# Optimization experiments

Measured on AMD Instinct MI355X. Metric: run time of the kernel, lower is better.

Reference implementation:

```python
import jax, jax.numpy as jnp
import numpy as np

B, N = 32, 196                  # batch, tokens (14x14 patches on all 4 scales)
CN = (64, 128, 256, 512)        # per-branch channel dims
H = 4                           # attention heads
KV = sum(CN)                    # 960
EPS = 1e-5                      # InstanceNorm2d default eps (affine=False)


def setup_inputs() -> dict:
    key = jax.random.key(0)
    ks = jax.random.split(key, 16)
    inp = {}
    for i, c in enumerate(CN):
        inp[f"emb{i+1}"] = jax.random.normal(ks[i], (B, N, c), dtype=jnp.float32)
    inp["emb_all"] = jnp.concatenate([inp[f"emb{i+1}"] for i in range(4)], axis=2)
    # per-head query weights (one Linear per head, bias=False): [H, out, in]
    for i, c in enumerate(CN):
        inp[f"Wq{i+1}"] = 0.02 * jax.random.normal(ks[4 + i], (H, c, c), dtype=jnp.float32)
    inp["Wk"] = 0.02 * jax.random.normal(ks[8], (H, KV, KV), dtype=jnp.float32)
    inp["Wv"] = 0.02 * jax.random.normal(ks[9], (H, KV, KV), dtype=jnp.float32)
    for i, c in enumerate(CN):
        inp[f"Wo{i+1}"] = 0.02 * jax.random.normal(ks[10 + i], (c, c), dtype=jnp.float32)
    return inp


def _branch(emb, Wq, K, V):
    # emb: [B,N,C], Wq: [H,C,C] -> Q^T: [B,H,C,N] (stack heads, transpose(-1,-2))
    Qt = jnp.einsum('bnd,hcd->bhcn', emb, Wq)
    # scores: [B,H,C,KV], scaled by sqrt(KV_size)
    s = jnp.einsum('bhcn,bhnk->bhck', Qt, K) * (1.0 / np.sqrt(KV))
    # InstanceNorm2d over spatial dims (C,KV) per (batch, head), no affine
    m = jnp.mean(s, axis=(2, 3), keepdims=True)
    v = jnp.var(s, axis=(2, 3), keepdims=True)
    s = (s - m) * jax.lax.rsqrt(v + EPS)
    p = jax.nn.softmax(s, axis=-1)              # softmax over KV dim (dim=3)
    # context = probs @ V^T -> [B,H,C,N]; permute(0,3,2,1).mean(dim=3) == mean over heads
    ctx = jnp.einsum('bhck,bhnk->bnc', p, V) / H  # [B,N,C]
    return ctx


def reference(emb1, emb2, emb3, emb4, emb_all,
              Wq1, Wq2, Wq3, Wq4, Wk, Wv, Wo1, Wo2, Wo3, Wo4):
    # per-head K/V projections of concatenated embedding: [B,H,N,KV]
    K = jnp.einsum('bnk,hok->bhno', emb_all, Wk)
    V = jnp.einsum('bnk,hok->bhno', emb_all, Wv)
    O1 = _branch(emb1, Wq1, K, V) @ Wo1.T
    O2 = _branch(emb2, Wq2, K, V) @ Wo2.T
    O3 = _branch(emb3, Wq3, K, V) @ Wo3.T
    O4 = _branch(emb4, Wq4, K, V) @ Wo4.T
    return (O1, O2, O3, O4)
```

## Files before the change

kernel.cpp:

```cpp
#include <hip/hip_runtime.h>
#include <math.h>

typedef __attribute__((ext_vector_type(8))) short bf16x8;
typedef __attribute__((ext_vector_type(4))) float f32x4;
typedef unsigned short u16;

__device__ __forceinline__ u16 f2bf(float f) {
  unsigned u = __float_as_uint(f);
  return (u16)((u + 0x7FFFu + ((u >> 16) & 1u)) >> 16);
}
__device__ __forceinline__ float bf2f(u16 h) {
  return __uint_as_float(((unsigned)h) << 16);
}

__device__ __forceinline__ void gload16(const u16* g, void* lds) {
  __builtin_amdgcn_global_load_lds(
      (const __attribute__((address_space(1))) unsigned int*)g,
      (__attribute__((address_space(3))) unsigned int*)lds, 16, 0, 0);
}

__device__ __forceinline__ void mfma_core(
    const u16* __restrict__ A, int lda,
    const u16* __restrict__ B, int ldb,
    int K, f32x4 (&acc)[4][4], u16* As, u16* Bs)
{
  const int tid = threadIdx.x;
  const int l = tid & 63, w = tid >> 6;
  const int srow = w * 16 + (l >> 2);
  const int kel  = (l & 3) * 8;
  char* AsB = (char*)As + w * 1024;
  char* BsB = (char*)Bs + w * 1024;
  const u16* Ap  = A + (size_t)srow * lda + kel;
  const u16* Ap2 = A + (size_t)(srow + 64) * lda + kel;
  const u16* Bp  = B + (size_t)srow * ldb + kel;
  const u16* Bp2 = B + (size_t)(srow + 64) * ldb + kel;
  const int wm = w >> 1, wn = w & 1;
  const int aoff = (wm * 64 + (l & 15)) * 32 + (l >> 4) * 8;
  const int boff = (wn * 64 + (l & 15)) * 32 + (l >> 4) * 8;
  for (int kb = 0; kb < K; kb += 32) {
    __syncthreads();
    gload16(Ap + kb,  AsB);
    gload16(Ap2 + kb, AsB + 4096);
    gload16(Bp + kb,  BsB);
    gload16(Bp2 + kb, BsB + 4096);
    __syncthreads();
    bf16x8 av[4], bv[4];
#pragma unroll
    for (int i = 0; i < 4; ++i) {
      av[i] = *(const bf16x8*)(As + aoff + i * 16 * 32);
      bv[i] = *(const bf16x8*)(Bs + boff + i * 16 * 32);
    }
#pragma unroll
    for (int i = 0; i < 4; ++i)
#pragma unroll
      for (int j = 0; j < 4; ++j)
        acc[i][j] = __builtin_amdgcn_mfma_f32_16x16x32_bf16(av[i], bv[j], acc[i][j], 0, 0, 0);
  }
}

__global__ __launch_bounds__(256) void k_cvt(
    const float* __restrict__ eall,
    const float* __restrict__ Wq1, const float* __restrict__ Wq2,
    const float* __restrict__ Wq3, const float* __restrict__ Wq4,
    const float* __restrict__ Wk, const float* __restrict__ Wv,
    const float* __restrict__ Wo1, const float* __restrict__ Wo2,
    const float* __restrict__ Wo3, const float* __restrict__ Wo4,
    u16* __restrict__ embA, u16* __restrict__ WkB, u16* __restrict__ WvB,
    u16* __restrict__ WqB, u16* __restrict__ WoB)
{
  long long idx = (long long)blockIdx.x * 256 + threadIdx.x;
  const float* src; u16* dst; int srcR, dstR, C; long long stride, off, loc;
  if (idx < 6881280LL)       { loc = idx;               src=eall; dst=embA; srcR=196; dstR=224;  C=960; stride=215040; off=0; }
  else if (idx < 10813440LL) { loc = idx - 6881280LL;   src=Wk;   dst=WkB;  srcR=960; dstR=1024; C=960; stride=983040; off=0; }
  else if (idx < 14745600LL) { loc = idx - 10813440LL;  src=Wv;   dst=WvB;  srcR=960; dstR=1024; C=960; stride=983040; off=0; }
  else if (idx < 14778368LL) { loc = idx - 14745600LL;  src=Wq1;  dst=WqB;  srcR=64;  dstR=128;  C=64;  stride=352256; off=0; }
  else if (idx < 14843904LL) { loc = idx - 14778368LL;  src=Wq2;  dst=WqB;  srcR=128; dstR=128;  C=128; stride=352256; off=8192; }
  else if (idx < 15106048LL) { loc = idx - 14843904LL;  src=Wq3;  dst=WqB;  srcR=256; dstR=256;  C=256; stride=352256; off=24576; }
  else if (idx < 16154624LL) { loc = idx - 15106048LL;  src=Wq4;  dst=WqB;  srcR=512; dstR=512;  C=512; stride=352256; off=90112; }
  else if (idx < 16162816LL) { loc = idx - 16154624LL;  src=Wo1;  dst=WoB;  srcR=64;  dstR=128;  C=64;  stride=0; off=0; }
  else if (idx < 16179200LL) { loc = idx - 16162816LL;  src=Wo2;  dst=WoB;  srcR=128; dstR=128;  C=128; stride=0; off=8192; }
  else if (idx < 16244736LL) { loc = idx - 16179200LL;  src=Wo3;  dst=WoB;  srcR=256; dstR=256;  C=256; stride=0; off=24576; }
  else if (idx < 16506880LL) { loc = idx - 16244736LL;  src=Wo4;  dst=WoB;  srcR=512; dstR=512;  C=512; stride=0; off=90112; }
  else return;
  const long long per = (long long)dstR * C;
  const int g = (int)(loc / per);
  const int r2 = (int)(loc % per);
  const int rr = r2 / C, c = r2 - rr * C;
  const float v = (rr < srcR) ? src[((long long)g * srcR + rr) * C + c] : 0.f;
  dst[g * stride + off + (long long)rr * C + c] = f2bf(v);
}

__global__ __launch_bounds__(256) void k_kt(const u16* __restrict__ embA,
    const u16* __restrict__ WkB, u16* __restrict__ Kt, int b0, int NB)
{
  __shared__ u16 As[128 * 32], Bs[128 * 32];
  const int h = blockIdx.z;
  const int m0 = blockIdx.y * 128, n0 = blockIdx.x * 128;
  const u16* A = WkB + (size_t)h * 1024 * 960 + (size_t)m0 * 960;
  const u16* B = embA + (size_t)(b0 * 224 + n0) * 960;
  f32x4 acc[4][4] = {};
  mfma_core(A, 960, B, 960, 960, acc, As, Bs);
  const int tid = threadIdx.x, l = tid & 63, w = tid >> 6, wm = w >> 1, wn = w & 1;
  u16* C = Kt + (size_t)h * 1024 * NB;
#pragma unroll
  for (int i = 0; i < 4; ++i) {
    const int gm0 = m0 + wm * 64 + i * 16 + (l >> 4) * 4;
#pragma unroll
    for (int j = 0; j < 4; ++j) {
      const int n = n0 + wn * 64 + j * 16 + (l & 15);
#pragma unroll
      for (int r = 0; r < 4; ++r)
        C[(size_t)(gm0 + r) * NB + n] = f2bf(acc[i][j][r]);
    }
  }
}

__global__ __launch_bounds__(256) void k_v(const u16* __restrict__ embA,
    const u16* __restrict__ WvB, u16* __restrict__ V, int b0, int NB)
{
  __shared__ u16 As[128 * 32], Bs[128 * 32];
  const int h = blockIdx.z;
  const int m0 = blockIdx.y * 128, n0 = blockIdx.x * 128;
  const u16* A = embA + (size_t)(b0 * 224 + m0) * 960;
  const u16* B = WvB + (size_t)h * 1024 * 960 + (size_t)n0 * 960;
  f32x4 acc[4][4] = {};
  mfma_core(A, 960, B, 960, 960, acc, As, Bs);
  const int tid = threadIdx.x, l = tid & 63, w = tid >> 6, wm = w >> 1, wn = w & 1;
#pragma unroll
  for (int i = 0; i < 4; ++i) {
    const int t0 = m0 + wm * 64 + i * 16 + (l >> 4) * 4;
#pragma unroll
    for (int r = 0; r < 4; ++r) {
      const int t = t0 + r;
      const int lb = t / 224, n = t - lb * 224;
      u16* C = V + ((size_t)(lb * 4 + h) * 256 + n) * 1024;
#pragma unroll
      for (int j = 0; j < 4; ++j) {
        const int col = n0 + wn * 64 + j * 16 + (l & 15);
        C[col] = f2bf(acc[i][j][r]);
      }
    }
  }
}

__global__ __launch_bounds__(256) void k_q(const u16* __restrict__ embA,
    const u16* __restrict__ WqB, u16* __restrict__ Qt, int b0, int NB)
{
  __shared__ u16 As[128 * 32], Bs[128 * 32];
  const int h = blockIdx.z;
  const int y = blockIdx.y;
  const int br = (y == 0) ? 0 : (y == 1) ? 1 : (y < 4) ? 2 : 3;
  const int mt = (y <= 1) ? 0 : (y < 4) ? (y - 2) : (y - 4);
  const int Ci = 64 << br;
  const int coff = (br == 0) ? 0 : (br == 1) ? 64 : (br == 2) ? 192 : 448;
  const int wqo = (br == 0) ? 0 : (br == 1) ? 8192 : (br == 2) ? 24576 : 90112;
  const int n0 = blockIdx.x * 128;
  const u16* A = WqB + (size_t)h * 352256 + wqo + (size_t)mt * 128 * Ci;
  const u16* B = embA + (size_t)(b0 * 224 + n0) * 960 + coff;
  f32x4 acc[4][4] = {};
  mfma_core(A, Ci, B, 960, Ci, acc, As, Bs);
  const int tid = threadIdx.x, l = tid & 63, w = tid >> 6, wm = w >> 1, wn = w & 1;
  u16* C = Qt + (size_t)h * 1024 * NB;
#pragma unroll
  for (int i = 0; i < 4; ++i) {
    const int lr0 = mt * 128 + wm * 64 + i * 16 + (l >> 4) * 4;
#pragma unroll
    for (int j = 0; j < 4; ++j) {
      const int n = n0 + wn * 64 + j * 16 + (l & 15);
#pragma unroll
      for (int r = 0; r < 4; ++r)
        if (lr0 + r < Ci)
          C[(size_t)(coff + lr0 + r) * NB + n] = f2bf(acc[i][j][r]);
    }
  }
}

#define TS_LD 72
__global__ __launch_bounds__(256) void k_gk(const u16* __restrict__ Kt,
                                            u16* __restrict__ Gk, int NB)
{
  __shared__ u16 TsA[128 * TS_LD], TsB[128 * TS_LD];
  const int z = blockIdx.z, lb = z >> 2, h = z & 3;
  const int n0a = blockIdx.y * 96, n0b = blockIdx.x * 96;
  const u16* Kz = Kt + (size_t)h * 1024 * NB + lb * 224;
  const int tid = threadIdx.x, l = tid & 63, w = tid >> 6, wm = w >> 1, wn = w & 1;
  f32x4 acc[4][4] = {};
  for (int o0 = 0; o0 < 1024; o0 += 64) {
    __syncthreads();
#pragma unroll
    for (int it = 0; it < 16; ++it) {
      const int e = it * 256 + tid;
      const int o = e >> 6, np = e & 63;
      const unsigned va = *(const unsigned*)(Kz + (size_t)(o0 + o) * NB + n0a + np * 2);
      const unsigned vb = *(const unsigned*)(Kz + (size_t)(o0 + o) * NB + n0b + np * 2);
      const int o8 = o >> 3, oe = o & 7;
      const int r0 = np * 2, r1 = r0 + 1;
      TsA[r0 * TS_LD + (((o8 ^ (r0 & 7)) << 3) | oe)] = (u16)(va & 0xffff);
      TsA[r1 * TS_LD + (((o8 ^ (r1 & 7)) << 3) | oe)] = (u16)(va >> 16);
      TsB[r0 * TS_LD + (((o8 ^ (r0 & 7)) << 3) | oe)] = (u16)(vb & 0xffff);
      TsB[r1 * TS_LD + (((o8 ^ (r1 & 7)) << 3) | oe)] = (u16)(vb >> 16);
    }
    __syncthreads();
#pragma unroll
    for (int ks = 0; ks < 2; ++ks) {
      bf16x8 av[4], bv[4];
#pragma unroll
      for (int i = 0; i < 4; ++i) {
        const int ra = wm * 64 + i * 16 + (l & 15);
        av[i] = *(const bf16x8*)(TsA + ra * TS_LD + (((ks * 4 + (l >> 4)) ^ (ra & 7)) << 3));
        const int rb = wn * 64 + i * 16 + (l & 15);
        bv[i] = *(const bf16x8*)(TsB + rb * TS_LD + (((ks * 4 + (l >> 4)) ^ (rb & 7)) << 3));
      }
#pragma unroll
      for (int i = 0; i < 4; ++i)
#pragma unroll
        for (int j = 0; j < 4; ++j)
          acc[i][j] = __builtin_amdgcn_mfma_f32_16x16x32_bf16(av[i], bv[j], acc[i][j], 0, 0, 0);
    }
  }
  u16* G = Gk + (size_t)z * 256 * 224;
#pragma unroll
  for (int i = 0; i < 4; ++i) {
    const int ra0 = n0a + wm * 64 + i * 16 + (l >> 4) * 4;
#pragma unroll
    for (int j = 0; j < 4; ++j) {
      const int cb = n0b + wn * 64 + j * 16 + (l & 15);
#pragma unroll
      for (int r = 0; r < 4; ++r)
        G[(size_t)(ra0 + r) * 224 + cb] = f2bf(acc[i][j][r]);
    }
  }
}

__global__ __launch_bounds__(256) void k_qgq(const u16* __restrict__ Qt,
    const u16* __restrict__ Gk, float* __restrict__ stats, int NB)
{
  __shared__ u16 As[128 * 32], Bs[128 * 32];
  __shared__ float sb[4];
  const int z = blockIdx.z, lb = z >> 2, h = z & 3;
  const int m0 = blockIdx.y * 128;
  const int tx = blockIdx.x;
  const int tid = threadIdx.x;
  if (tid < 4) sb[tid] = 0.f;
  const u16* A = Qt + (size_t)h * 1024 * NB + (size_t)m0 * NB + lb * 224;
  const u16* B = Gk + (size_t)z * 256 * 224 + (size_t)(tx * 96) * 224;
  f32x4 acc[4][4] = {};
  mfma_core(A, NB, B, 224, 224, acc, As, Bs);
  const int l = tid & 63, w = tid >> 6, wm = w >> 1, wn = w & 1;
  const u16* Qbase = Qt + (size_t)h * 1024 * NB + lb * 224;
  float part[4]; int pbr[4]; bool ok[4];
#pragma unroll
  for (int i = 0; i < 4; ++i) {
    const int gm0 = m0 + wm * 64 + i * 16 + (l >> 4) * 4;
    pbr[i] = (gm0 < 64) ? 0 : (gm0 < 192) ? 1 : (gm0 < 448) ? 2 : 3;
    ok[i] = (gm0 < 960);
    float s = 0.f;
    if (ok[i]) {
#pragma unroll
      for (int j = 0; j < 4; ++j) {
        const int col = tx * 96 + wn * 64 + j * 16 + (l & 15);
        if (tx == 1 && col < 128) continue;
#pragma unroll
        for (int r = 0; r < 4; ++r)
          s += acc[i][j][r] * bf2f(Qbase[(size_t)(gm0 + r) * NB + col]);
      }
    }
    part[i] = s;
  }
  __syncthreads();
#pragma unroll
  for (int i = 0; i < 4; ++i)
    if (ok[i]) atomicAdd(&sb[pbr[i]], part[i]);
  __syncthreads();
  if (tid < 4) atomicAdd(stats + (size_t)z * 4 + tid, sb[tid]);
}

__global__ __launch_bounds__(256, 2) void k_att(
    const u16* __restrict__ Qt, const u16* __restrict__ Kt,
    const u16* __restrict__ V, const float* __restrict__ stats,
    u16* __restrict__ ctxh, int NB)
{
  __shared__ u16 smem[39744];
  __shared__ float rsum[64];

  const int z = blockIdx.x, ct = blockIdx.y;
  const int lb = z >> 2, h = z & 3;
  const int c0 = ct * 64;
  const int tid = threadIdx.x, l = tid & 63, w = tid >> 6;
  const int wm = w >> 1, wn = w & 1;
  const int br = (c0 < 64) ? 0 : (c0 < 192) ? 1 : (c0 < 448) ? 2 : 3;
  const float scale = 0.03227486121839514f;
  const float cnt = (float)(64 << br) * 960.f;
  const float var = stats[(size_t)z * 4 + br] * scale * scale / cnt;
  const float cs = scale * rsqrtf(var + 1e-5f);

  const u16* Qz = Qt + (size_t)h * 1024 * NB + (size_t)c0 * NB + lb * 224;
  const u16* Kz = Kt + (size_t)h * 1024 * NB + lb * 224;
  const u16* Vz = V + (size_t)z * 256 * 1024;

  bf16x8 qa[2][7];
#pragma unroll
  for (int i = 0; i < 2; ++i)
#pragma unroll
    for (int ks = 0; ks < 7; ++ks)
      qa[i][ks] = *(const bf16x8*)(Qz + (size_t)(wm * 32 + i * 16 + (l & 15)) * NB
                                   + ks * 32 + (l >> 4) * 8);
  if (tid < 64) rsum[tid] = 0.f;

  const u16* kp[4];
#pragma unroll
  for (int c = 0; c < 4; ++c) {
    const int e = (c * 4 + w) * 512 + l * 8;
    const int row = e / 232, col = e - row * 232;
    kp[c] = Kz + (size_t)row * NB + col;
  }
  const u16* vp[5];
#pragma unroll
  for (int c = 0; c < 5; ++c) {
    const int e = (c * 4 + w) * 512 + l * 8;
    const int row = e / 40, col = e - row * 40;
    vp[c] = Vz + (size_t)row * 1024 + col;
  }
  u16* Ps = smem + 37184;

#pragma unroll
  for (int c = 0; c < 4; ++c) { gload16(kp[c], (char*)(smem) + (c * 4 + w) * 1024); kp[c] += (size_t)32 * NB; }
#pragma unroll
  for (int c = 0; c < 5; ++c) { gload16(vp[c], (char*)(smem + 16704) + (c * 4 + w) * 1024); vp[c] += 32; }
  __syncthreads();

  f32x4 cacc[7][2] = {};
  float rp[2][4] = {};
  int cur = 0;

  for (int oc = 0; oc < 30; ++oc) {
    const int koff = cur ? 8352 : 0;
    const int voff = cur ? 26944 : 16704;
    const int koff2 = cur ? 0 : 8352;
    const int voff2 = cur ? 16704 : 26944;
    if (oc < 29) {
#pragma unroll
      for (int c = 0; c < 4; ++c) { gload16(kp[c], (char*)(smem + koff2) + (c * 4 + w) * 1024); kp[c] += (size_t)32 * NB; }
#pragma unroll
      for (int c = 0; c < 5; ++c) { gload16(vp[c], (char*)(smem + voff2) + (c * 4 + w) * 1024); vp[c] += 32; }
    }
    const u16* Ks = smem + koff;
    const u16* Vs = smem + voff;
    f32x4 sacc[2] = {};
#pragma unroll
    for (int ks = 0; ks < 7; ++ks) {
      const bf16x8 kb = *(const bf16x8*)(Ks + (wn * 16 + (l & 15)) * 232 + ks * 32 + (l >> 4) * 8);
#pragma unroll
      for (int i = 0; i < 2; ++i)
        sacc[i] = __builtin_amdgcn_mfma_f32_16x16x32_bf16(qa[i][ks], kb, sacc[i], 0, 0, 0);
    }
#pragma unroll
    for (int i = 0; i < 2; ++i)
#pragma unroll
      for (int r = 0; r < 4; ++r) {
        const float p = __expf(sacc[i][r] * cs);
        rp[i][r] += p;
        Ps[(wm * 32 + i * 16 + (l >> 4) * 4 + r) * 40 + wn * 16 + (l & 15)] = f2bf(p);
      }
    asm volatile("s_waitcnt lgkmcnt(0)" ::: "memory");
    __builtin_amdgcn_s_barrier();
    __builtin_amdgcn_sched_barrier(0);
    bf16x8 pv[2];
#pragma unroll
    for (int j = 0; j < 2; ++j)
      pv[j] = *(const bf16x8*)(Ps + (wn * 32 + j * 16 + (l & 15)) * 40 + (l >> 4) * 8);
#pragma unroll
    for (int i2 = 0; i2 < 7; ++i2) {
      const bf16x8 av = *(const bf16x8*)(Vs + (wm * 112 + i2 * 16 + (l & 15)) * 40 + (l >> 4) * 8);
#pragma unroll
      for (int j = 0; j < 2; ++j)
        cacc[i2][j] = __builtin_amdgcn_mfma_f32_16x16x32_bf16(av, pv[j], cacc[i2][j], 0, 0, 0);
    }
    asm volatile("s_waitcnt vmcnt(0) lgkmcnt(0)" ::: "memory");
    __builtin_amdgcn_s_barrier();
    __builtin_amdgcn_sched_barrier(0);
    cur ^= 1;
  }
#pragma unroll
  for (int i = 0; i < 2; ++i)
#pragma unroll
    for (int r = 0; r < 4; ++r) {
      float v = rp[i][r];
      v += __shfl_xor(v, 1); v += __shfl_xor(v, 2);
      v += __shfl_xor(v, 4); v += __shfl_xor(v, 8);
      if ((l & 15) == 0) atomicAdd(&rsum[wm * 32 + i * 16 + (l >> 4) * 4 + r], v);
    }
  __syncthreads();
  float inv[2];
#pragma unroll
  for (int j = 0; j < 2; ++j)
    inv[j] = 1.f / rsum[wn * 32 + j * 16 + (l & 15)];

  u16* Cs = smem;
  u16* dst = ctxh + (size_t)z * 229376 + c0;
#pragma unroll
  for (int pass = 0; pass < 2; ++pass) {
    __syncthreads();
    if (wm == pass) {
#pragma unroll
      for (int i2 = 0; i2 < 7; ++i2)
#pragma unroll
        for (int j = 0; j < 2; ++j)
#pragma unroll
          for (int r = 0; r < 4; ++r)
            Cs[(i2 * 16 + (l >> 4) * 4 + r) * 72 + wn * 32 + j * 16 + (l & 15)]
                = f2bf(cacc[i2][j][r] * inv[j]);
    }
    __syncthreads();
    for (int u = tid; u < 112 * 8; u += 256) {
      const int row = u >> 3, c8 = u & 7;
      *(uint4*)(dst + (size_t)(pass * 112 + row) * 1024 + c8 * 8) =
          *(const uint4*)(Cs + row * 72 + c8 * 8);
    }
  }
}

__global__ __launch_bounds__(256) void k_ctxred(const u16* __restrict__ ctxh,
    u16* __restrict__ ctx, int Bc)
{
  const long long i8 = ((long long)blockIdx.x * 256 + threadIdx.x) * 8;
  if (i8 >= (long long)Bc * 229376) return;
  const int lb = (int)(i8 / 229376);
  const int off = (int)(i8 - (long long)lb * 229376);
  const u16* p = ctxh + (size_t)lb * 4 * 229376 + off;
  float s[8] = {};
#pragma unroll
  for (int h = 0; h < 4; ++h) {
    bf16x8 v = *(const bf16x8*)(p + (size_t)h * 229376);
#pragma unroll
    for (int i = 0; i < 8; ++i) s[i] += bf2f((u16)v[i]);
  }
  bf16x8 o;
#pragma unroll
  for (int i = 0; i < 8; ++i) o[i] = (short)f2bf(s[i] * 0.25f);
  *(bf16x8*)(ctx + (size_t)lb * 262144 + off) = o;
}

__global__ __launch_bounds__(256) void k_o(const u16* __restrict__ ctx,
    const u16* __restrict__ WoB, float* __restrict__ out, int b0)
{
  __shared__ u16 As[128 * 32], Bs[128 * 32];
  const int lb = blockIdx.z;
  const int x = blockIdx.x;
  const int br = (x == 0) ? 0 : (x == 1) ? 1 : (x < 4) ? 2 : 3;
  const int nt = (x <= 1) ? 0 : (x < 4) ? (x - 2) : (x - 4);
  const int Ci = 64 << br;
  const int coff = (br == 0) ? 0 : (br == 1) ? 64 : (br == 2) ? 192 : 448;
  const int woo = (br == 0) ? 0 : (br == 1) ? 8192 : (br == 2) ? 24576 : 90112;
  const long long ob = (br == 0) ? 0LL : (br == 1) ? 401408LL : (br == 2) ? 1204224LL : 2809856LL;
  const int m0 = blockIdx.y * 128;
  const u16* A = ctx + (size_t)lb * 262144 + (size_t)m0 * 1024 + coff;
  const u16* B = WoB + woo + (size_t)nt * 128 * Ci;
  f32x4 acc[4][4] = {};
  mfma_core(A, 1024, B, Ci, Ci, acc, As, Bs);
  const int tid = threadIdx.x, l = tid & 63, w = tid >> 6, wm = w >> 1, wn = w & 1;
  float* O = out + ob;
  const int gb = b0 + lb;
#pragma unroll
  for (int i = 0; i < 4; ++i) {
    const int row0 = m0 + wm * 64 + i * 16 + (l >> 4) * 4;
#pragma unroll
    for (int j = 0; j < 4; ++j) {
      const int cg = nt * 128 + wn * 64 + j * 16 + (l & 15);
#pragma unroll
      for (int r = 0; r < 4; ++r) {
        const int row = row0 + r;
        if (row < 196 && cg < Ci)
          O[((size_t)gb * 196 + row) * Ci + cg] = acc[i][j][r];
      }
    }
  }
}

extern "C" void kernel_launch(void* const* d_in, const int* in_sizes, int n_in,
                              void* d_out, int out_size, void* d_ws, size_t ws_size,
                              hipStream_t stream)
{
  const float* eall = (const float*)d_in[4];
  const float* Wq1 = (const float*)d_in[5];
  const float* Wq2 = (const float*)d_in[6];
  const float* Wq3 = (const float*)d_in[7];
  const float* Wq4 = (const float*)d_in[8];
  const float* Wk  = (const float*)d_in[9];
  const float* Wv  = (const float*)d_in[10];
  const float* Wo1 = (const float*)d_in[11];
  const float* Wo2 = (const float*)d_in[12];
  const float* Wo3 = (const float*)d_in[13];
  const float* Wo4 = (const float*)d_in[14];
  float* out = (float*)d_out;

  char* p = (char*)d_ws;
  auto alloc = [&](size_t bytes) -> void* {
    void* r = p; p += (bytes + 255) & ~(size_t)255; return r;
  };
  u16* embA = (u16*)alloc((size_t)7168 * 960 * 2);
  u16* WkB  = (u16*)alloc((size_t)4 * 1024 * 960 * 2);
  u16* WvB  = (u16*)alloc((size_t)4 * 1024 * 960 * 2);
  u16* WqB  = (u16*)alloc((size_t)4 * 352256 * 2);
  u16* WoB  = (u16*)alloc((size_t)352256 * 2);
  const size_t persist = (size_t)(p - (char*)d_ws);
  const size_t perLB = (size_t)1835008 * 2 + 2097152 + 458752 + 1835008 + 524288 + 64 + 2048;
  int Bc = 8;
  if      (persist + 32 * perLB <= ws_size) Bc = 32;
  else if (persist + 16 * perLB <= ws_size) Bc = 16;
  const int NB = Bc * 224;
  const int Z = Bc * 4;

  u16* Kt  = (u16*)alloc((size_t)4 * 1024 * NB * 2);
  u16* Qt  = (u16*)alloc((size_t)4 * 1024 * NB * 2);
  u16* V   = (u16*)alloc((size_t)Bc * 4 * 256 * 1024 * 2);
  u16* Gk  = (u16*)alloc((size_t)Bc * 4 * 256 * 224 * 2);
  u16* ctxh = (u16*)alloc((size_t)Bc * 4 * 229376 * 2);
  u16* ctx = (u16*)alloc((size_t)Bc * 262144 * 2);
  float* stats = (float*)alloc((size_t)Bc * 16 * 4);

  const dim3 blk(256);
  k_cvt<<<dim3(64480), blk, 0, stream>>>(eall, Wq1, Wq2, Wq3, Wq4, Wk, Wv,
                                         Wo1, Wo2, Wo3, Wo4,
                                         embA, WkB, WvB, WqB, WoB);

  const int NT = NB / 128;
  for (int b0 = 0; b0 < 32; b0 += Bc) {
    (void)hipMemsetAsync(stats, 0, (size_t)Bc * 16 * 4, stream);
    k_kt<<<dim3(NT, 8, 4), blk, 0, stream>>>(embA, WkB, Kt, b0, NB);
    k_v <<<dim3(8, NT, 4), blk, 0, stream>>>(embA, WvB, V, b0, NB);
    k_q <<<dim3(NT, 8, 4), blk, 0, stream>>>(embA, WqB, Qt, b0, NB);
    k_gk<<<dim3(2, 2, Z), blk, 0, stream>>>(Kt, Gk, NB);
    k_qgq<<<dim3(2, 8, Z), blk, 0, stream>>>(Qt, Gk, stats, NB);
    k_att<<<dim3(Z, 15), blk, 0, stream>>>(Qt, Kt, V, stats, ctxh, NB);
    k_ctxred<<<dim3((Bc * 229376 / 8 + 255) / 256), blk, 0, stream>>>(ctxh, ctx, Bc);
    k_o <<<dim3(8, 2, Bc), blk, 0, stream>>>(ctx, WoB, out, b0);
  }
}
```

Baseline: 819.2 us.

## Drop K/V double buffering in attention kernel to fit three blocks per CU

Replaces the double-buffered K/V LDS staging in k_att with a single buffer that is loaded synchronously at the top of each iteration. LDS use drops from about 79KB to about 38KB, and launch bounds rise to 3 blocks per CU so more waves can hide latency. The cost is losing the prefetch overlap inside each block: every iteration now waits on global loads before compute and adds extra barriers. Register pressure may also go up under the tighter launch bound.

```diff
diff --git a/kernel.cpp b/kernel.cpp
--- a/kernel.cpp
+++ b/kernel.cpp
@@ -275,12 +275,12 @@
   if (tid < 4) atomicAdd(stats + (size_t)z * 4 + tid, sb[tid]);
 }
 
-__global__ __launch_bounds__(256, 2) void k_att(
+__global__ __launch_bounds__(256, 3) void k_att(
     const u16* __restrict__ Qt, const u16* __restrict__ Kt,
     const u16* __restrict__ V, const float* __restrict__ stats,
     u16* __restrict__ ctxh, int NB)
 {
-  __shared__ u16 smem[39744];
+  __shared__ u16 smem[18944];
   __shared__ float rsum[64];
 
   const int z = blockIdx.x, ct = blockIdx.y;
@@ -309,47 +309,39 @@
 
   const u16* kp[4];
 #pragma unroll
-  for (int c = 0; c < 4; ++c) {
-    const int e = (c * 4 + w) * 512 + l * 8;
-    const int row = e / 232, col = e - row * 232;
-    kp[c] = Kz + (size_t)row * NB + col;
+  for (int s = 0; s < 4; ++s) {
+    const int e16 = s * 256 + tid;
+    const int row = e16 / 29, col = (e16 - row * 29) * 8;
+    kp[s] = Kz + (size_t)row * NB + col;
   }
   const u16* vp[5];
 #pragma unroll
-  for (int c = 0; c < 5; ++c) {
-    const int e = (c * 4 + w) * 512 + l * 8;
-    const int row = e / 40, col = e - row * 40;
-    vp[c] = Vz + (size_t)row * 1024 + col;
-  }
-  u16* Ps = smem + 37184;
-
-#pragma unroll
-  for (int c = 0; c < 4; ++c) { gload16(kp[c], (char*)(smem) + (c * 4 + w) * 1024); kp[c] += (size_t)32 * NB; }
-#pragma unroll
-  for (int c = 0; c < 5; ++c) { gload16(vp[c], (char*)(smem + 16704) + (c * 4 + w) * 1024); vp[c] += 32; }
-  __syncthreads();
+  for (int s = 0; s < 5; ++s) {
+    const int e16 = s * 256 + tid;
+    const int row = e16 / 5, col = (e16 - row * 5) * 8;
+    vp[s] = Vz + (size_t)row * 1024 + col;
+  }
+  u16* Ps = smem + 16384;
+  const int wb = (tid & 192) * 16;
 
   f32x4 cacc[7][2] = {};
   float rp[2][4] = {};
-  int cur = 0;
 
   for (int oc = 0; oc < 30; ++oc) {
-    const int koff = cur ? 8352 : 0;
-    const int voff = cur ? 26944 : 16704;
-    const int koff2 = cur ? 0 : 8352;
-    const int voff2 = cur ? 16704 : 26944;
-    if (oc < 29) {
-#pragma unroll
-      for (int c = 0; c < 4; ++c) { gload16(kp[c], (char*)(smem + koff2) + (c * 4 + w) * 1024); kp[c] += (size_t)32 * NB; }
-#pragma unroll
-      for (int c = 0; c < 5; ++c) { gload16(vp[c], (char*)(smem + voff2) + (c * 4 + w) * 1024); vp[c] += 32; }
-    }
-    const u16* Ks = smem + koff;
-    const u16* Vs = smem + voff;
+    __syncthreads();
+#pragma unroll
+    for (int s = 0; s < 3; ++s) { gload16(kp[s], (char*)smem + s * 4096 + wb); kp[s] += (size_t)32 * NB; }
+    if (tid < 160)                { gload16(kp[3], (char*)smem + 12288 + wb); }
+    kp[3] += (size_t)32 * NB;
+#pragma unroll
+    for (int s = 0; s < 4; ++s) { gload16(vp[s], (char*)smem + 14848 + s * 4096 + wb); vp[s] += 32; }
+    if (tid < 96)               { gload16(vp[4], (char*)smem + 14848 + 16384 + wb); }
+    vp[4] += 32;
+    __syncthreads();
     f32x4 sacc[2] = {};
 #pragma unroll
     for (int ks = 0; ks < 7; ++ks) {
-      const bf16x8 kb = *(const bf16x8*)(Ks + (wn * 16 + (l & 15)) * 232 + ks * 32 + (l >> 4) * 8);
+      const bf16x8 kb = *(const bf16x8*)(smem + (wn * 16 + (l & 15)) * 232 + ks * 32 + (l >> 4) * 8);
 #pragma unroll
       for (int i = 0; i < 2; ++i)
         sacc[i] = __builtin_amdgcn_mfma_f32_16x16x32_bf16(qa[i][ks], kb, sacc[i], 0, 0, 0);
@@ -362,25 +354,20 @@
         rp[i][r] += p;
         Ps[(wm * 32 + i * 16 + (l >> 4) * 4 + r) * 40 + wn * 16 + (l & 15)] = f2bf(p);
       }
-    asm volatile("s_waitcnt lgkmcnt(0)" ::: "memory");
-    __builtin_amdgcn_s_barrier();
-    __builtin_amdgcn_sched_barrier(0);
+    __syncthreads();
     bf16x8 pv[2];
 #pragma unroll
     for (int j = 0; j < 2; ++j)
       pv[j] = *(const bf16x8*)(Ps + (wn * 32 + j * 16 + (l & 15)) * 40 + (l >> 4) * 8);
 #pragma unroll
     for (int i2 = 0; i2 < 7; ++i2) {
-      const bf16x8 av = *(const bf16x8*)(Vs + (wm * 112 + i2 * 16 + (l & 15)) * 40 + (l >> 4) * 8);
+      const bf16x8 av = *(const bf16x8*)(smem + 7424 + (wm * 112 + i2 * 16 + (l & 15)) * 40 + (l >> 4) * 8);
 #pragma unroll
       for (int j = 0; j < 2; ++j)
         cacc[i2][j] = __builtin_amdgcn_mfma_f32_16x16x32_bf16(av, pv[j], cacc[i2][j], 0, 0, 0);
     }
-    asm volatile("s_waitcnt vmcnt(0) lgkmcnt(0)" ::: "memory");
-    __builtin_amdgcn_s_barrier();
-    __builtin_amdgcn_sched_barrier(0);
-    cur ^= 1;
-  }
+  }
+  __syncthreads();
 #pragma unroll
   for (int i = 0; i < 2; ++i)
 #pragma unroll
```

Measured after the change: 825.1 us. About the same (+0.7%).
